# Kernel optimization log

Measured on AMD Instinct MI355X. Metric: run time of the kernel, lower is better.

## Reference

```python
import jax, jax.numpy as jnp
import numpy as np

L = 768
Z_DIM = 128
C = 32
EPS = 1e-5


def _layer_norm(x, w, b):
    mu = jnp.mean(x, axis=-1, keepdims=True)
    var = jnp.mean(jnp.square(x - mu), axis=-1, keepdims=True)
    return (x - mu) * jax.lax.rsqrt(var + EPS) * w + b


def setup_inputs() -> dict:
    key = jax.random.key(0)
    ks = jax.random.split(key, 12)
    s_z = 1.0 / np.sqrt(Z_DIM)
    s_c = 1.0 / np.sqrt(C)
    return {
        "z": jax.random.normal(ks[0], (L, L, Z_DIM), dtype=jnp.float32),
        "norm_w": jnp.ones((Z_DIM,), jnp.float32),
        "norm_b": jnp.zeros((Z_DIM,), jnp.float32),
        "onorm_w": jnp.ones((C,), jnp.float32),
        "onorm_b": jnp.zeros((C,), jnp.float32),
        "a_w": jax.random.normal(ks[1], (C, Z_DIM), jnp.float32) * s_z,
        "a_b": jnp.zeros((C,), jnp.float32),
        "ag_w": jax.random.normal(ks[2], (C, Z_DIM), jnp.float32) * s_z,
        "ag_b": jnp.zeros((C,), jnp.float32),
        "g_w": jax.random.normal(ks[3], (Z_DIM, Z_DIM), jnp.float32) * s_z,
        "g_b": jnp.zeros((Z_DIM,), jnp.float32),
        "o_w": jax.random.normal(ks[4], (Z_DIM, C), jnp.float32) * s_c,
        "o_b": jnp.zeros((Z_DIM,), jnp.float32),
    }


def reference(z, norm_w, norm_b, onorm_w, onorm_b, a_w, a_b, ag_w, ag_b, g_w, g_b, o_w, o_b):
    zn = _layer_norm(z, norm_w, norm_b)                       # [L,L,Z]
    a = (zn @ a_w.T + a_b) * jax.nn.sigmoid(zn @ ag_w.T + ag_b)  # [L,L,C]
    # source computes b with the same (a) projections -> b == a
    o = jnp.einsum('ilc,jlc->ijc', a, a)                      # [L,L,C]
    o = _layer_norm(o, onorm_w, onorm_b)
    o = o @ o_w.T + o_b                                        # [L,L,Z]
    o = o * jax.nn.sigmoid(zn @ g_w.T + g_b)
    return o
```

## Files before the change

kernel.cpp:

```cpp
#include <hip/hip_runtime.h>
#include <math.h>


#define LDIM 768
#define LL   (768 * 768)
#define ZD   128
#define CD   32

typedef __bf16 bf16x8 __attribute__((ext_vector_type(8)));
typedef float  f32x4  __attribute__((ext_vector_type(4)));

__device__ __forceinline__ ushort f2bf(float f) {
    __bf16 h = (__bf16)f;
    return __builtin_bit_cast(ushort, h);
}
__device__ __forceinline__ float bf2f(ushort u) {
    return __builtin_bit_cast(float, ((unsigned)u) << 16);
}
__device__ __forceinline__ float sigm(float x) {
    return __builtin_amdgcn_rcpf(1.0f + __expf(-x));
}

__global__ __launch_bounds__(256) void k0_wfrag(
    const float* __restrict__ aw, const float* __restrict__ agw,
    const float* __restrict__ gw, ushort* __restrict__ wfrag)
{
    const int f = blockIdx.x * 256 + threadIdx.x;
    if (f >= 12 * 4 * 64) return;
    const int n4 = f >> 6, lane = f & 63;
    const int n = n4 >> 2, kk = n4 & 3;
    const int fr = lane & 15, hi = lane >> 4;
    const int ch = n * 16 + fr;
    const int k0 = kk * 32 + hi * 8;
    const float* src = (ch < 32) ? (aw + ch * ZD)
                     : (ch < 64) ? (agw + (ch - 32) * ZD)
                                 : (gw + (ch - 64) * ZD);
    union { ushort us[8]; uint4 q; } pk;
    #pragma unroll
    for (int j = 0; j < 8; ++j) pk.us[j] = f2bf(src[k0 + j]);
    *(uint4*)&wfrag[(size_t)f * 8] = pk.q;
}

__global__ __launch_bounds__(256) void k1_ln_proj(
    const float* __restrict__ z, const float* __restrict__ nw, const float* __restrict__ nb,
    const ushort* __restrict__ wfrag,
    const float* __restrict__ ab, const float* __restrict__ agb, const float* __restrict__ gb,
    ushort* __restrict__ a_t, ushort* __restrict__ gate)
{
    __shared__ ushort zn[64][136];
    __shared__ ushort gl[64][136];

    const int tid = threadIdx.x;
    const int lane = tid & 63, wave = tid >> 6;
    const int fr = lane & 15, hi = lane >> 4;

    const int t0 = (wave < 2) ? wave     : 6 + (wave - 2) * 3;
    const int t1 = (wave < 2) ? wave + 2 : t0 + 1;
    const int t2 = (wave < 2) ? wave + 4 : t0 + 2;

    bf16x8 bv0[4], bv1[4], bv2[4];
    {
        const ushort* wl = wfrag + (size_t)lane * 8;
        #pragma unroll
        for (int kk = 0; kk < 4; ++kk) {
            bv0[kk] = *(const bf16x8*)(wl + (size_t)(t0 * 4 + kk) * 512);
            bv1[kk] = *(const bf16x8*)(wl + (size_t)(t1 * 4 + kk) * 512);
            bv2[kk] = *(const bf16x8*)(wl + (size_t)(t2 * 4 + kk) * 512);
        }
    }

    float abv = 0.f, agbv = 0.f, gbv0 = 0.f, gbv1 = 0.f, gbv2;
    if (wave < 2) {
        abv  = ab[wave * 16 + fr];
        agbv = agb[wave * 16 + fr];
        gbv2 = gb[t2 * 16 - 64 + fr];
    } else {
        gbv0 = gb[t0 * 16 - 64 + fr];
        gbv1 = gb[t1 * 16 - 64 + fr];
        gbv2 = gb[t2 * 16 - 64 + fr];
    }

    const size_t blockrow = (size_t)blockIdx.x * 256;
    const int lr = tid >> 2, seg = tid & 3;

    float4 zreg[8];
    {
        const float4* zp = (const float4*)(z + (blockrow + lr) * ZD + seg * 32);
        #pragma unroll
        for (int q = 0; q < 8; ++q) zreg[q] = zp[q];
    }

    for (int c = 0; c < 4; ++c) {
        __syncthreads();

        {
            float v[32];
            #pragma unroll
            for (int q = 0; q < 8; ++q) {
                v[q * 4 + 0] = zreg[q].x; v[q * 4 + 1] = zreg[q].y;
                v[q * 4 + 2] = zreg[q].z; v[q * 4 + 3] = zreg[q].w;
            }
            float s = 0.f, ss = 0.f;
            #pragma unroll
            for (int e = 0; e < 32; ++e) { s += v[e]; ss += v[e] * v[e]; }
            s += __shfl_xor(s, 1); ss += __shfl_xor(ss, 1);
            s += __shfl_xor(s, 2); ss += __shfl_xor(ss, 2);
            const float mu  = s * (1.f / 128.f);
            const float var = ss * (1.f / 128.f) - mu * mu;
            const float rs  = rsqrtf(var + 1e-5f);
            union { ushort u[32]; uint4 q4[4]; } pk;
            #pragma unroll
            for (int e = 0; e < 32; ++e) {
                const int k = seg * 32 + e;
                pk.u[e] = f2bf((v[e] - mu) * rs * nw[k] + nb[k]);
            }
            #pragma unroll
            for (int q = 0; q < 4; ++q)
                *(uint4*)&zn[lr][seg * 32 + q * 8] = pk.q4[q];
        }

        if (c < 3) {
            const float4* zp = (const float4*)(z + (blockrow + (c + 1) * 64 + lr) * ZD + seg * 32);
            #pragma unroll
            for (int q = 0; q < 8; ++q) zreg[q] = zp[q];
        }
        __syncthreads();

        f32x4 acc0[4], acc1[4], acc2[4];
        #pragma unroll
        for (int m = 0; m < 4; ++m) {
            acc0[m] = (f32x4){0.f, 0.f, 0.f, 0.f};
            acc1[m] = (f32x4){0.f, 0.f, 0.f, 0.f};
            acc2[m] = (f32x4){0.f, 0.f, 0.f, 0.f};
        }
        #pragma unroll
        for (int m = 0; m < 4; ++m) {
            bf16x8 afm[4];
            #pragma unroll
            for (int kk = 0; kk < 4; ++kk)
                afm[kk] = *(const bf16x8*)&zn[m * 16 + fr][kk * 32 + hi * 8];
            #pragma unroll
            for (int kk = 0; kk < 4; ++kk) {
                acc0[m] = __builtin_amdgcn_mfma_f32_16x16x32_bf16(afm[kk], bv0[kk], acc0[m], 0, 0, 0);
                acc1[m] = __builtin_amdgcn_mfma_f32_16x16x32_bf16(afm[kk], bv1[kk], acc1[m], 0, 0, 0);
                acc2[m] = __builtin_amdgcn_mfma_f32_16x16x32_bf16(afm[kk], bv2[kk], acc2[m], 0, 0, 0);
            }
        }

        const size_t rb = blockrow + (size_t)c * 64;
        if (wave < 2) {
            const int ch = wave * 16 + fr;
            #pragma unroll
            for (int m = 0; m < 4; ++m) {
                union { ushort u[4]; uint2 d; } pk;
                #pragma unroll
                for (int q = 0; q < 4; ++q)
                    pk.u[q] = f2bf((acc0[m][q] + abv) * sigm(acc1[m][q] + agbv));
                *(uint2*)&a_t[(size_t)ch * LL + rb + m * 16 + hi * 4] = pk.d;
            }
            const int gch = t2 * 16 - 64 + fr;
            #pragma unroll
            for (int m = 0; m < 4; ++m)
                #pragma unroll
                for (int q = 0; q < 4; ++q)
                    gl[m * 16 + hi * 4 + q][gch] = f2bf(sigm(acc2[m][q] + gbv2));
        } else {
            const int g0 = t0 * 16 - 64 + fr;
            const int g1 = t1 * 16 - 64 + fr;
            const int g2 = t2 * 16 - 64 + fr;
            #pragma unroll
            for (int m = 0; m < 4; ++m)
                #pragma unroll
                for (int q = 0; q < 4; ++q) {
                    const int row = m * 16 + hi * 4 + q;
                    gl[row][g0] = f2bf(sigm(acc0[m][q] + gbv0));
                    gl[row][g1] = f2bf(sigm(acc1[m][q] + gbv1));
                    gl[row][g2] = f2bf(sigm(acc2[m][q] + gbv2));
                }
        }
        __syncthreads();

        #pragma unroll
        for (int it = 0; it < 4; ++it) {
            const int idx = it * 256 + tid;
            const int r = idx >> 4, cq = idx & 15;
            *(uint4*)&gate[(rb + r) * ZD + cq * 8] = *(const uint4*)&gl[r][cq * 8];
        }
    }
}

__global__ __launch_bounds__(256) void k2_einsum(
    const ushort* __restrict__ a_t, float* __restrict__ obuf)
{
    __shared__ ushort As[2][64][32];
    __shared__ ushort Bs[2][64][32];

    const int tid = threadIdx.x;
    const int c = blockIdx.y;
    int p = blockIdx.x, bi = 0;
    while (p >= 12 - bi) { p -= 12 - bi; ++bi; }
    const int bj = bi + p;
    const int i0 = bi * 64, j0 = bj * 64;
    const ushort* base = a_t + (size_t)c * LL;

    const int srow = tid >> 2, scol = (tid & 3) * 8;
    const ushort* gA = base + (size_t)(i0 + srow) * LDIM + scol;
    const ushort* gB = base + (size_t)(j0 + srow) * LDIM + scol;

    const int wave = tid >> 6, lane = tid & 63;
    const int wi = (wave >> 1) * 32, wj = (wave & 1) * 32;
    const int fr = lane & 15, k8 = (lane >> 4) * 8;

    f32x4 acc[2][2];
    #pragma unroll
    for (int m = 0; m < 2; ++m)
        #pragma unroll
        for (int n = 0; n < 2; ++n)
            acc[m][n] = (f32x4){0.f, 0.f, 0.f, 0.f};

    auto stage = [&](int b, int kc) {
        __builtin_amdgcn_global_load_lds(
            (const uint*)(gA + kc * 32), (uint*)&As[b][srow][scol], 16, 0, 0);
        __builtin_amdgcn_global_load_lds(
            (const uint*)(gB + kc * 32), (uint*)&Bs[b][srow][scol], 16, 0, 0);
    };

    stage(0, 0);
    __syncthreads();
    for (int kc = 0; kc < 24; ++kc) {
        const int cur = kc & 1;
        if (kc + 1 < 24) stage(cur ^ 1, kc + 1);

        bf16x8 av[2], bv[2];
        #pragma unroll
        for (int m = 0; m < 2; ++m)
            av[m] = *(const bf16x8*)&As[cur][wi + m * 16 + fr][k8];
        #pragma unroll
        for (int n = 0; n < 2; ++n)
            bv[n] = *(const bf16x8*)&Bs[cur][wj + n * 16 + fr][k8];

        #pragma unroll
        for (int m = 0; m < 2; ++m)
            #pragma unroll
            for (int n = 0; n < 2; ++n)
                acc[m][n] = __builtin_amdgcn_mfma_f32_16x16x32_bf16(
                    av[m], bv[n], acc[m][n], 0, 0, 0);
        __syncthreads();
    }

    float* ob = obuf + (size_t)c * LL;
    #pragma unroll
    for (int m = 0; m < 2; ++m)
        #pragma unroll
        for (int n = 0; n < 2; ++n) {
            #pragma unroll
            for (int q = 0; q < 4; ++q) {
                const int row = i0 + wi + m * 16 + (lane >> 4) * 4 + q;
                const int col = j0 + wj + n * 16 + fr;
                ob[(size_t)row * LDIM + col] = acc[m][n][q];
            }
            if (bi != bj) {
                const int mrow = j0 + wj + n * 16 + fr;
                const int mcol = i0 + wi + m * 16 + (lane >> 4) * 4;
                float4 w;
                w.x = acc[m][n][0]; w.y = acc[m][n][1];
                w.z = acc[m][n][2]; w.w = acc[m][n][3];
                *(float4*)&ob[(size_t)mrow * LDIM + mcol] = w;
            }
        }
}

__global__ __launch_bounds__(256) void k3_out(
    const float* __restrict__ obuf,
    const float* __restrict__ onw, const float* __restrict__ onb,
    const float* __restrict__ ow,  const float* __restrict__ obias,
    const ushort* __restrict__ gate, float* __restrict__ out)
{
    __shared__ union { float Ol[64][40]; float Res[64][132]; } u;
    __shared__ ushort An[64][36];
    __shared__ ushort Bw[128][36];

    const int tid = threadIdx.x;
    const size_t rowbase = (size_t)blockIdx.x * 64;

    {
        const int jj = tid & 63, cg = tid >> 6;
        const size_t off = rowbase + jj;
        #pragma unroll
        for (int cc = 0; cc < 8; ++cc) {
            const int ch = cg * 8 + cc;
            u.Ol[jj][ch] = obuf[(size_t)ch * LL + off];
        }
    }
    {
        const int r = tid >> 1, h = tid & 1;
        const float* src = ow + r * CD + h * 16;
        union { ushort us[16]; uint4 q[2]; } pk;
        #pragma unroll
        for (int e = 0; e < 16; ++e) pk.us[e] = f2bf(src[e]);
        *(uint4*)&Bw[r][h * 16]     = pk.q[0];
        *(uint4*)&Bw[r][h * 16 + 8] = pk.q[1];
    }
    __syncthreads();

    {
        const int r = tid >> 2, seg = tid & 3;
        float v[8];
        #pragma unroll
        for (int e = 0; e < 8; ++e) v[e] = u.Ol[r][seg * 8 + e];
        float s = 0.f, ss = 0.f;
        #pragma unroll
        for (int e = 0; e < 8; ++e) { s += v[e]; ss += v[e] * v[e]; }
        s += __shfl_xor(s, 1); ss += __shfl_xor(ss, 1);
        s += __shfl_xor(s, 2); ss += __shfl_xor(ss, 2);
        const float mu  = s * (1.f / 32.f);
        const float var = ss * (1.f / 32.f) - mu * mu;
        const float rs  = rsqrtf(var + 1e-5f);
        union { ushort us[8]; uint4 q; } pk;
        #pragma unroll
        for (int e = 0; e < 8; ++e) {
            const int c = seg * 8 + e;
            pk.us[e] = f2bf((v[e] - mu) * rs * onw[c] + onb[c]);
        }
        *(uint4*)&An[r][seg * 8] = pk.q;
    }
    __syncthreads();

    const int lane = tid & 63, wave = tid >> 6;
    const int fr = lane & 15, hi = lane >> 4;
    const int wrow = wave * 16;

    const bf16x8 af = *(const bf16x8*)&An[wrow + fr][hi * 8];
    f32x4 acc[8];
    #pragma unroll
    for (int n = 0; n < 8; ++n) {
        const bf16x8 bv = *(const bf16x8*)&Bw[n * 16 + fr][hi * 8];
        acc[n] = __builtin_amdgcn_mfma_f32_16x16x32_bf16(
            af, bv, (f32x4){0.f, 0.f, 0.f, 0.f}, 0, 0, 0);
    }

    #pragma unroll
    for (int n = 0; n < 8; ++n) {
        const int ch = n * 16 + fr;
        const float obv = obias[ch];
        #pragma unroll
        for (int q = 0; q < 4; ++q)
            u.Res[wrow + hi * 4 + q][ch] = acc[n][q] + obv;
    }
    __syncthreads();

    #pragma unroll
    for (int it = 0; it < 8; ++it) {
        const int idx = it * 256 + tid;
        const int r = idx >> 5, cq = (idx & 31) * 4;
        float4 v4 = *(const float4*)&u.Res[r][cq];
        union { uint2 d; ushort us[4]; } g;
        g.d = *(const uint2*)&gate[(rowbase + r) * ZD + cq];
        v4.x *= bf2f(g.us[0]); v4.y *= bf2f(g.us[1]);
        v4.z *= bf2f(g.us[2]); v4.w *= bf2f(g.us[3]);
        *(float4*)&out[(rowbase + r) * ZD + cq] = v4;
    }
}

extern "C" void kernel_launch(void* const* d_in, const int* in_sizes, int n_in,
                              void* d_out, int out_size, void* d_ws, size_t ws_size,
                              hipStream_t stream) {
    (void)in_sizes; (void)n_in; (void)out_size; (void)ws_size;
    const float* z   = (const float*)d_in[0];
    const float* nw  = (const float*)d_in[1];
    const float* nb  = (const float*)d_in[2];
    const float* onw = (const float*)d_in[3];
    const float* onb = (const float*)d_in[4];
    const float* aw  = (const float*)d_in[5];
    const float* ab  = (const float*)d_in[6];
    const float* agw = (const float*)d_in[7];
    const float* agb = (const float*)d_in[8];
    const float* gw  = (const float*)d_in[9];
    const float* gb  = (const float*)d_in[10];
    const float* ow  = (const float*)d_in[11];
    const float* ob  = (const float*)d_in[12];

    char* ws = (char*)d_ws;
    ushort* a_t  = (ushort*)ws;
    ushort* gate = (ushort*)(ws + 37748736);
    float*  obuf = (float*)(ws + 37748736 + 150994944);
    ushort* wfrag = (ushort*)obuf;

    k0_wfrag<<<12, 256, 0, stream>>>(aw, agw, gw, wfrag);
    k1_ln_proj<<<LL / 256, 256, 0, stream>>>(z, nw, nb, wfrag, ab, agb, gb,
                                             a_t, gate);
    k2_einsum<<<dim3(78, 32), 256, 0, stream>>>(a_t, obuf);
    k3_out<<<LL / 64, 256, 0, stream>>>(obuf, onw, onb, ow, ob, gate,
                                        (float*)d_out);
}
```

Before: 287.6 us.

## Store einsum output in bf16 and write gate directly to global memory

The einsum intermediate between k2 and k3 is now stored as bf16 instead of fp32, which halves that buffer's write and read traffic (about 75 MB in fp32). k3 reads pairs of bf16 values and widens them into shared memory. k1 drops its shared-memory staging of the gate tile and the extra barrier, writing scattered 2-byte values straight to global memory. The gate writes lose coalescing, and rounding the einsum output to bf16 before the layer norm reduces precision.

```diff
diff --git a/kernel.cpp b/kernel.cpp
--- a/kernel.cpp
+++ b/kernel.cpp
@@ -48,7 +48,6 @@
     ushort* __restrict__ a_t, ushort* __restrict__ gate)
 {
     __shared__ ushort zn[64][136];
-    __shared__ ushort gl[64][136];
 
     const int tid = threadIdx.x;
     const int lane = tid & 63, wave = tid >> 6;
@@ -163,7 +162,8 @@
             for (int m = 0; m < 4; ++m)
                 #pragma unroll
                 for (int q = 0; q < 4; ++q)
-                    gl[m * 16 + hi * 4 + q][gch] = f2bf(sigm(acc2[m][q] + gbv2));
+                    gate[(rb + m * 16 + hi * 4 + q) * ZD + gch] =
+                        f2bf(sigm(acc2[m][q] + gbv2));
         } else {
             const int g0 = t0 * 16 - 64 + fr;
             const int g1 = t1 * 16 - 64 + fr;
@@ -172,25 +172,17 @@
             for (int m = 0; m < 4; ++m)
                 #pragma unroll
                 for (int q = 0; q < 4; ++q) {
-                    const int row = m * 16 + hi * 4 + q;
-                    gl[row][g0] = f2bf(sigm(acc0[m][q] + gbv0));
-                    gl[row][g1] = f2bf(sigm(acc1[m][q] + gbv1));
-                    gl[row][g2] = f2bf(sigm(acc2[m][q] + gbv2));
+                    const size_t row = rb + m * 16 + hi * 4 + q;
+                    gate[row * ZD + g0] = f2bf(sigm(acc0[m][q] + gbv0));
+                    gate[row * ZD + g1] = f2bf(sigm(acc1[m][q] + gbv1));
+                    gate[row * ZD + g2] = f2bf(sigm(acc2[m][q] + gbv2));
                 }
         }
-        __syncthreads();
-
-        #pragma unroll
-        for (int it = 0; it < 4; ++it) {
-            const int idx = it * 256 + tid;
-            const int r = idx >> 4, cq = idx & 15;
-            *(uint4*)&gate[(rb + r) * ZD + cq * 8] = *(const uint4*)&gl[r][cq * 8];
-        }
     }
 }
 
 __global__ __launch_bounds__(256) void k2_einsum(
-    const ushort* __restrict__ a_t, float* __restrict__ obuf)
+    const ushort* __restrict__ a_t, ushort* __restrict__ obuf16)
 {
     __shared__ ushort As[2][64][32];
     __shared__ ushort Bs[2][64][32];
@@ -248,7 +240,7 @@
         __syncthreads();
     }
 
-    float* ob = obuf + (size_t)c * LL;
+    ushort* ob = obuf16 + (size_t)c * LL;
     #pragma unroll
     for (int m = 0; m < 2; ++m)
         #pragma unroll
@@ -257,21 +249,21 @@
             for (int q = 0; q < 4; ++q) {
                 const int row = i0 + wi + m * 16 + (lane >> 4) * 4 + q;
                 const int col = j0 + wj + n * 16 + fr;
-                ob[(size_t)row * LDIM + col] = acc[m][n][q];
+                ob[(size_t)row * LDIM + col] = f2bf(acc[m][n][q]);
             }
             if (bi != bj) {
                 const int mrow = j0 + wj + n * 16 + fr;
                 const int mcol = i0 + wi + m * 16 + (lane >> 4) * 4;
-                float4 w;
-                w.x = acc[m][n][0]; w.y = acc[m][n][1];
-                w.z = acc[m][n][2]; w.w = acc[m][n][3];
-                *(float4*)&ob[(size_t)mrow * LDIM + mcol] = w;
+                union { ushort u[4]; uint2 d; } pk;
+                #pragma unroll
+                for (int q = 0; q < 4; ++q) pk.u[q] = f2bf(acc[m][n][q]);
+                *(uint2*)&ob[(size_t)mrow * LDIM + mcol] = pk.d;
             }
         }
 }
 
 __global__ __launch_bounds__(256) void k3_out(
-    const float* __restrict__ obuf,
+    const ushort* __restrict__ obuf16,
     const float* __restrict__ onw, const float* __restrict__ onb,
     const float* __restrict__ ow,  const float* __restrict__ obias,
     const ushort* __restrict__ gate, float* __restrict__ out)
@@ -281,16 +273,16 @@
     __shared__ ushort Bw[128][36];
 
     const int tid = threadIdx.x;
+    const int lane = tid & 63, wave = tid >> 6;
     const size_t rowbase = (size_t)blockIdx.x * 64;
 
-    {
-        const int jj = tid & 63, cg = tid >> 6;
-        const size_t off = rowbase + jj;
-        #pragma unroll
-        for (int cc = 0; cc < 8; ++cc) {
-            const int ch = cg * 8 + cc;
-            u.Ol[jj][ch] = obuf[(size_t)ch * LL + off];
-        }
+    #pragma unroll
+    for (int cc = 0; cc < 4; ++cc) {
+        const int ch = wave * 8 + cc * 2 + (lane >> 5);
+        const int r2 = (lane & 31) * 2;
+        const uint uu = *(const uint*)&obuf16[(size_t)ch * LL + rowbase + r2];
+        u.Ol[r2][ch]     = bf2f((ushort)(uu & 0xffff));
+        u.Ol[r2 + 1][ch] = bf2f((ushort)(uu >> 16));
     }
     {
         const int r = tid >> 1, h = tid & 1;
@@ -326,7 +318,6 @@
     }
     __syncthreads();
 
-    const int lane = tid & 63, wave = tid >> 6;
     const int fr = lane & 15, hi = lane >> 4;
     const int wrow = wave * 16;
 
@@ -381,15 +372,15 @@
     const float* ob  = (const float*)d_in[12];
 
     char* ws = (char*)d_ws;
-    ushort* a_t  = (ushort*)ws;
-    ushort* gate = (ushort*)(ws + 37748736);
-    float*  obuf = (float*)(ws + 37748736 + 150994944);
-    ushort* wfrag = (ushort*)obuf;
+    ushort* a_t    = (ushort*)ws;
+    ushort* gate   = (ushort*)(ws + 37748736);
+    ushort* obuf16 = (ushort*)(ws + 188743680);
+    ushort* wfrag  = (ushort*)(ws + 226492416);
 
     k0_wfrag<<<12, 256, 0, stream>>>(aw, agw, gw, wfrag);
     k1_ln_proj<<<LL / 256, 256, 0, stream>>>(z, nw, nb, wfrag, ab, agb, gb,
                                              a_t, gate);
-    k2_einsum<<<dim3(78, 32), 256, 0, stream>>>(a_t, obuf);
-    k3_out<<<LL / 64, 256, 0, stream>>>(obuf, onw, onb, ow, ob, gate,
+    k2_einsum<<<dim3(78, 32), 256, 0, stream>>>(a_t, obuf16);
+    k3_out<<<LL / 64, 256, 0, stream>>>(obuf16, onw, onb, ow, ob, gate,
                                         (float*)d_out);
 }
```

Result: slower. 314.6 us (+9.4%).
